# Optimization experiments

Hardware: AMD Instinct MI355X
Metric: run time of the kernel (lower is better)

The kernel has to match this reference:

```python
import jax, jax.numpy as jnp
import numpy as np

V, D, H, DH, DI, L = 10000, 512, 8, 64, 2048, 12
B, S = 4, 1024
MAX_KLEN = 1024 + 0 + 512  # tgt_len + ext_len + mem_len
EPS = 1e-5
STD = 0.02


def setup_inputs() -> dict:
    key = jax.random.key(0)
    ks = jax.random.split(key, 10)
    data = jax.random.randint(ks[0], (B, S), 0, V)
    word_emb = jax.random.normal(ks[1], (V, D), jnp.float32) * STD
    pos_emb = jax.random.normal(ks[2], (MAX_KLEN, D), jnp.float32) * STD
    Wq = jax.random.normal(ks[3], (L, H * DH, D), jnp.float32) * STD
    Wkv = jax.random.normal(ks[4], (L, 2 * H * DH, D), jnp.float32) * STD
    Wo = jax.random.normal(ks[5], (L, D, H * DH), jnp.float32) * STD
    ln1_g = jnp.ones((L, D), jnp.float32)
    ln1_b = jnp.zeros((L, D), jnp.float32)
    W1 = jax.random.normal(ks[6], (L, DI, D), jnp.float32) * STD
    b1 = jnp.zeros((L, DI), jnp.float32)
    W2 = jax.random.normal(ks[7], (L, D, DI), jnp.float32) * STD
    b2 = jnp.zeros((L, D), jnp.float32)
    ln2_g = jnp.ones((L, D), jnp.float32)
    ln2_b = jnp.zeros((L, D), jnp.float32)
    out_b = jnp.zeros((V,), jnp.float32)  # out_layer weight is tied to word_emb
    return dict(data=data, word_emb=word_emb, pos_emb=pos_emb, Wq=Wq, Wkv=Wkv,
                Wo=Wo, ln1_g=ln1_g, ln1_b=ln1_b, W1=W1, b1=b1, W2=W2, b2=b2,
                ln2_g=ln2_g, ln2_b=ln2_b, out_b=out_b)


def _layernorm(x, g, b):
    m = jnp.mean(x, axis=-1, keepdims=True)
    v = jnp.mean((x - m) ** 2, axis=-1, keepdims=True)
    return (x - m) * jax.lax.rsqrt(v + EPS) * g + b


def reference(data, word_emb, pos_emb, Wq, Wkv, Wo, ln1_g, ln1_b,
              W1, b1, W2, b2, ln2_g, ln2_b, out_b):
    # mems start empty -> mlen = 0, klen = qlen, standard causal mask.
    h = word_emb[data] + pos_emb[:S][None, :, :]      # [B, S, D]
    mask = jnp.triu(jnp.ones((S, S), bool), 1)        # True above diagonal
    scale = 1.0 / np.sqrt(DH)

    def layer(h, p):
        wq, wkv, wo, g1, bl1, w1, bf1, w2, bf2, g2, bl2 = p
        q = (h @ wq.T).reshape(B, S, H, DH)
        k, v = jnp.split(h @ wkv.T, 2, axis=-1)
        k = k.reshape(B, S, H, DH)
        v = v.reshape(B, S, H, DH)
        sc = jnp.einsum('bqhd,bkhd->bhqk', q, k) * scale
        sc = jnp.where(mask[None, None], -jnp.inf, sc)
        p_attn = jax.nn.softmax(sc, axis=-1)           # [B, H, S, S] materialized
        av = jnp.einsum('bhqk,bkhd->bqhd', p_attn, v).reshape(B, S, H * DH)
        h = _layernorm(h + av @ wo.T, g1, bl1)         # post-LN (pre_lnorm=False)
        ff = jax.nn.relu(h @ w1.T + bf1) @ w2.T + bf2
        h = _layernorm(h + ff, g2, bl2)
        return h, None

    h, _ = jax.lax.scan(layer, h,
                        (Wq, Wkv, Wo, ln1_g, ln1_b, W1, b1, W2, b2, ln2_g, ln2_b))
    logits = h @ word_emb.T + out_b                    # tied output projection
    return logits                                      # [B, S, V]
```

## Files before the change

### kernel.cpp

```cpp
#include <hip/hip_runtime.h>

#define VV 10000
#define DD 512
#define HH 8
#define DH 64
#define DI 2048
#define LL 12
#define BB 4
#define SS 1024
#define TT (BB * SS)


typedef __attribute__((ext_vector_type(8))) short bhalf8;
typedef __attribute__((ext_vector_type(16))) float f32x16;

__device__ __forceinline__ void split_bf16(float x, unsigned short& h, unsigned short& l)
{
    unsigned int u = __float_as_uint(x);
    unsigned int r = (u + 0x7FFFu + ((u >> 16) & 1u)) & 0xFFFF0000u;
    h = (unsigned short)(r >> 16);
    float lf = x - __uint_as_float(r);
    unsigned int ul = __float_as_uint(lf);
    l = (unsigned short)((ul + 0x7FFFu + ((ul >> 16) & 1u)) >> 16);
}

__global__ __launch_bounds__(256) void convsplit(
    const float* __restrict__ src, unsigned short* __restrict__ hi,
    unsigned short* __restrict__ lo, int n4)
{
    int stride = gridDim.x * 256;
    for (int i = blockIdx.x * 256 + threadIdx.x; i < n4; i += stride) {
        float4 v = ((const float4*)src)[i];
        ushort4 h, l;
        split_bf16(v.x, h.x, l.x);
        split_bf16(v.y, h.y, l.y);
        split_bf16(v.z, h.z, l.z);
        split_bf16(v.w, h.w, l.w);
        ((ushort4*)hi)[i] = h;
        ((ushort4*)lo)[i] = l;
    }
}

__global__ __launch_bounds__(256) void embed_kernel(
    const int* __restrict__ data, const float* __restrict__ we,
    const float* __restrict__ pe, float* __restrict__ h,
    unsigned short* __restrict__ hhi, unsigned short* __restrict__ hlo)
{
    int tok = blockIdx.x;
    int tid = threadIdx.x;
    int idx = data[tok];
    int s = tok & (SS - 1);
    size_t base = (size_t)tok * DD;
    size_t wb = (size_t)idx * DD;
    size_t pb = (size_t)s * DD;
    float a = we[wb + tid] + pe[pb + tid];
    float b = we[wb + 256 + tid] + pe[pb + 256 + tid];
    h[base + tid] = a;
    h[base + 256 + tid] = b;
    unsigned short hx, lx;
    split_bf16(a, hx, lx); hhi[base + tid] = hx;       hlo[base + tid] = lx;
    split_bf16(b, hx, lx); hhi[base + 256 + tid] = hx; hlo[base + 256 + tid] = lx;
}

template<int BN, int EPI, bool SWZ>
__global__ __launch_bounds__(256) void gemm_mfma(
    const unsigned short* __restrict__ Ahp, const unsigned short* __restrict__ Alp,
    const unsigned short* __restrict__ Whp, const unsigned short* __restrict__ Wlp,
    const float* __restrict__ bias, float* __restrict__ C,
    unsigned short* __restrict__ Chp, unsigned short* __restrict__ Clp,
    unsigned short* __restrict__ Vhp, unsigned short* __restrict__ Vlp,
    int N, int K)
{
    constexpr int FN  = BN / 64;
    constexpr int BT  = BN * 128;
    constexpr int NBG = BN / 8;
    constexpr int NGRP = 32 + 2 * NBG;
    constexpr int PW  = NGRP / 4;
    __shared__ __align__(16) char smem[32768 + 2 * BT];

    int bx = blockIdx.x, by = blockIdx.y;
    if (SWZ) {
        int id = by * 79 + bx;
        int t  = (id & 7) * 316 + (id >> 3);
        if (t < 2240) { int c = t / 320, r = t - c * 320; by = r / 10; bx = c * 10 + r % 10; }
        else          { int r = t - 2240;                 by = r / 9;  bx = 70 + r % 9; }
    }

    const int tid   = threadIdx.x;
    const int lane  = tid & 63;
    const int wid   = tid >> 6;
    const int wm    = wid >> 1;
    const int wn    = wid & 1;
    const int laneM = lane & 31;
    const int laneK = lane >> 5;
    const int m0    = by * 128;
    const int n0    = bx * BN;
    const int srow8 = lane >> 3;
    const int sslot = lane & 7;

    const int dAl = (int)(Alp - Ahp);
    const int dW  = (int)(Whp - Ahp);
    const int dWl = (int)(Wlp - Ahp);
    int offs[PW];
    int ldso[PW];
    #pragma unroll
    for (int t = 0; t < PW; ++t) {
        int g = wid * PW + t;
        if (g < 32) {
            int row = (g & 15) * 8 + srow8;
            offs[t] = (g < 16 ? 0 : dAl) + (m0 + row) * K + sslot * 8;
            ldso[t] = ((g >> 4) << 14) + sslot * 2048 + ((row ^ sslot) << 4);
        } else {
            int d = g - 32;
            int row = (d & (NBG - 1)) * 8 + srow8;
            int n = n0 + row;
            n = (n < N) ? n : (N - 1);
            offs[t] = (d < NBG ? dW : dWl) + n * K + sslot * 8;
            ldso[t] = 32768 + ((d < NBG) ? 0 : BT)
                    + sslot * (BN * 16) + ((row ^ sslot) << 4);
        }
    }

    f32x16 acc[2][FN];
    #pragma unroll
    for (int i = 0; i < 2; ++i)
        #pragma unroll
        for (int j = 0; j < FN; ++j)
            #pragma unroll
            for (int r = 0; r < 16; ++r) acc[i][j][r] = 0.f;

    bhalf8 rbuf[PW];
    #pragma unroll
    for (int t = 0; t < PW; ++t)
        rbuf[t] = *(const bhalf8*)(Ahp + offs[t]);

    for (int k0 = 0; k0 < K; k0 += 64) {
        __syncthreads();
        #pragma unroll
        for (int t = 0; t < PW; ++t)
            *(bhalf8*)(smem + ldso[t]) = rbuf[t];
        __syncthreads();

        if (k0 + 64 < K) {
            #pragma unroll
            for (int t = 0; t < PW; ++t)
                rbuf[t] = *(const bhalf8*)(Ahp + offs[t] + k0 + 64);
        }

        #pragma unroll
        for (int kb = 0; kb < 4; ++kb) {
            const int slot = kb * 2 + laneK;
            bhalf8 ah[2], al[2], bh[FN], bl[FN];
            #pragma unroll
            for (int i = 0; i < 2; ++i) {
                int row = wm * 64 + i * 32 + laneM;
                int off = slot * 2048 + ((row ^ slot) << 4);
                ah[i] = *(const bhalf8*)(smem + off);
                al[i] = *(const bhalf8*)(smem + 16384 + off);
            }
            #pragma unroll
            for (int j = 0; j < FN; ++j) {
                int row = wn * (BN / 2) + j * 32 + laneM;
                int off = 32768 + slot * (BN * 16) + ((row ^ slot) << 4);
                bh[j] = *(const bhalf8*)(smem + off);
                bl[j] = *(const bhalf8*)(smem + BT + off);
            }
            #pragma unroll
            for (int i = 0; i < 2; ++i)
                #pragma unroll
                for (int j = 0; j < FN; ++j) {
                    acc[i][j] = __builtin_amdgcn_mfma_f32_32x32x16_bf16(ah[i], bh[j], acc[i][j], 0, 0, 0);
                    acc[i][j] = __builtin_amdgcn_mfma_f32_32x32x16_bf16(ah[i], bl[j], acc[i][j], 0, 0, 0);
                    acc[i][j] = __builtin_amdgcn_mfma_f32_32x32x16_bf16(al[i], bh[j], acc[i][j], 0, 0, 0);
                }
        }
    }

    #pragma unroll
    for (int j = 0; j < FN; ++j) {
        int ncol = n0 + wn * (BN / 2) + j * 32 + laneM;
        bool nok = (ncol < N);
        float bv = 0.f;
        if (EPI == 1 || EPI == 2) { if (nok) bv = bias[ncol]; }
        #pragma unroll
        for (int i = 0; i < 2; ++i) {
            #pragma unroll
            for (int r = 0; r < 16; ++r) {
                int mrow = m0 + wm * 64 + i * 32 + (r & 3) + ((r >> 2) << 3) + laneK * 4;
                float v = acc[i][j][r] + bv;
                if (EPI == 2) v = fmaxf(v, 0.f);
                if (nok) {
                    if (EPI == 2 || EPI == 3) {
                        unsigned short hx, lx;
                        split_bf16(v, hx, lx);
                        Chp[(size_t)mrow * N + ncol] = hx;
                        Clp[(size_t)mrow * N + ncol] = lx;
                    } else if (EPI == 4) {
                        unsigned short hx, lx;
                        split_bf16(v, hx, lx);
                        if (ncol < 512) {
                            Chp[(size_t)mrow * 512 + ncol] = hx;
                            Clp[(size_t)mrow * 512 + ncol] = lx;
                        } else {
                            Vhp[(size_t)(ncol - 512) * TT + mrow] = hx;
                            Vlp[(size_t)(ncol - 512) * TT + mrow] = lx;
                        }
                    } else {
                        C[(size_t)mrow * N + ncol] = v;
                    }
                }
            }
        }
    }
}

__global__ __launch_bounds__(128) void flash_mfma(
    const unsigned short* __restrict__ qhp, const unsigned short* __restrict__ qlp,
    const unsigned short* __restrict__ khp, const unsigned short* __restrict__ klp,
    const unsigned short* __restrict__ vthp, const unsigned short* __restrict__ vtlp,
    unsigned short* __restrict__ avh, unsigned short* __restrict__ avl)
{
    __shared__ __align__(16) char lds[50176];

    const int qt  = 15 - (int)blockIdx.x;
    const int hh  = blockIdx.y;
    const int b   = blockIdx.z;
    const int tid = threadIdx.x;
    const int lane  = tid & 63;
    const int wq    = tid >> 6;
    const int laneM = lane & 31;
    const int laneK = lane >> 5;
    const int q0    = qt * 64;

    bhalf8 Qh[4], Ql[4];
    {
        size_t qoff = (size_t)(b * SS + q0 + 32 * wq + laneM) * 512 + hh * 64 + 8 * laneK;
        #pragma unroll
        for (int ks = 0; ks < 4; ++ks) {
            Qh[ks] = *(const bhalf8*)(qhp + qoff + 16 * ks);
            Ql[ks] = *(const bhalf8*)(qlp + qoff + 16 * ks);
        }
    }

    f32x16 O0, O1;
    #pragma unroll
    for (int r = 0; r < 16; ++r) { O0[r] = 0.f; O1[r] = 0.f; }
    float mrun = -1e30f, lrun = 0.f;

    const int srow  = tid >> 1;
    const int shalf = tid & 1;
    float* Pl = (float*)(lds + 32768 + wq * 8704);

    for (int kt = 0; kt <= qt; ++kt) {
        __syncthreads();
        {
            size_t kbase = (size_t)(b * SS + kt * 64 + srow) * 512 + hh * 64 + 32 * shalf;
            size_t vbase = (size_t)(hh * 64 + srow) * TT + b * SS + kt * 64 + 32 * shalf;
            bhalf8 k0[4], k1[4], v0[4], v1[4];
            #pragma unroll
            for (int j = 0; j < 4; ++j) {
                k0[j] = *(const bhalf8*)(khp  + kbase + 8 * j);
                k1[j] = *(const bhalf8*)(klp  + kbase + 8 * j);
                v0[j] = *(const bhalf8*)(vthp + vbase + 8 * j);
                v1[j] = *(const bhalf8*)(vtlp + vbase + 8 * j);
            }
            int ob = srow * 128 + 64 * shalf;
            int sw = (srow & 7) << 4;
            #pragma unroll
            for (int j = 0; j < 4; ++j) {
                int o = (ob + 16 * j) ^ sw;
                *(bhalf8*)(lds + o)         = k0[j];
                *(bhalf8*)(lds + 8192 + o)  = k1[j];
                *(bhalf8*)(lds + 16384 + o) = v0[j];
                *(bhalf8*)(lds + 24576 + o) = v1[j];
            }
        }
        __syncthreads();

        f32x16 s0, s1;
        #pragma unroll
        for (int r = 0; r < 16; ++r) { s0[r] = 0.f; s1[r] = 0.f; }
        __builtin_amdgcn_s_setprio(1);
        #pragma unroll
        for (int ks = 0; ks < 4; ++ks) {
            int db = 32 * ks + 16 * laneK;
            int o0 = (laneM * 128 + db) ^ ((laneM & 7) << 4);
            int r1 = 32 + laneM;
            int o1 = (r1 * 128 + db) ^ ((r1 & 7) << 4);
            bhalf8 kh0 = *(const bhalf8*)(lds + o0);
            bhalf8 kl0 = *(const bhalf8*)(lds + 8192 + o0);
            bhalf8 kh1 = *(const bhalf8*)(lds + o1);
            bhalf8 kl1 = *(const bhalf8*)(lds + 8192 + o1);
            s0 = __builtin_amdgcn_mfma_f32_32x32x16_bf16(kh0, Qh[ks], s0, 0, 0, 0);
            s0 = __builtin_amdgcn_mfma_f32_32x32x16_bf16(kh0, Ql[ks], s0, 0, 0, 0);
            s0 = __builtin_amdgcn_mfma_f32_32x32x16_bf16(kl0, Qh[ks], s0, 0, 0, 0);
            s1 = __builtin_amdgcn_mfma_f32_32x32x16_bf16(kh1, Qh[ks], s1, 0, 0, 0);
            s1 = __builtin_amdgcn_mfma_f32_32x32x16_bf16(kh1, Ql[ks], s1, 0, 0, 0);
            s1 = __builtin_amdgcn_mfma_f32_32x32x16_bf16(kl1, Qh[ks], s1, 0, 0, 0);
        }
        __builtin_amdgcn_s_setprio(0);

        #pragma unroll
        for (int r = 0; r < 16; ++r) { s0[r] *= 0.125f; s1[r] *= 0.125f; }

        if (kt == qt) {
            int qrel = 32 * wq + laneM;
            #pragma unroll
            for (int r = 0; r < 16; ++r) {
                int krel = (r & 3) + ((r >> 2) << 3) + 4 * laneK;
                if (krel > qrel)      s0[r] = -1e30f;
                if (krel + 32 > qrel) s1[r] = -1e30f;
            }
        }

        float mx = s0[0];
        #pragma unroll
        for (int r = 1; r < 16; ++r) mx = fmaxf(mx, s0[r]);
        #pragma unroll
        for (int r = 0; r < 16; ++r) mx = fmaxf(mx, s1[r]);
        mx = fmaxf(mx, __shfl_xor(mx, 32));
        float mn = fmaxf(mrun, mx);
        float alpha = __expf(mrun - mn);
        mrun = mn;
        float rs = 0.f;
        #pragma unroll
        for (int r = 0; r < 16; ++r) {
            float p0 = __expf(s0[r] - mn);
            float p1 = __expf(s1[r] - mn);
            s0[r] = p0; s1[r] = p1;
            rs += p0 + p1;
        }
        rs += __shfl_xor(rs, 32);
        lrun = lrun * alpha + rs;
        #pragma unroll
        for (int r = 0; r < 16; ++r) { O0[r] *= alpha; O1[r] *= alpha; }

        #pragma unroll
        for (int r = 0; r < 16; ++r) {
            int krel = (r & 3) + ((r >> 2) << 3) + 4 * laneK;
            Pl[laneM * 68 + krel]      = s0[r];
            Pl[laneM * 68 + 32 + krel] = s1[r];
        }
        __asm__ volatile("s_waitcnt lgkmcnt(0)" ::: "memory");
        __builtin_amdgcn_sched_barrier(0);

        #pragma unroll
        for (int ks = 0; ks < 4; ++ks) {
            const float* pr = &Pl[laneM * 68 + 16 * ks + 8 * laneK];
            float4 pa = *(const float4*)pr;
            float4 pb = *(const float4*)(pr + 4);
            float pv[8] = {pa.x, pa.y, pa.z, pa.w, pb.x, pb.y, pb.z, pb.w};
            bhalf8 ph, plo;
            #pragma unroll
            for (int i = 0; i < 8; ++i) {
                unsigned u = __float_as_uint(pv[i]);
                ph[i] = (short)(u >> 16);
                float lf = pv[i] - __uint_as_float(u & 0xFFFF0000u);
                plo[i] = (short)(__float_as_uint(lf) >> 16);
            }
            int db = 32 * ks + 16 * laneK;
            __builtin_amdgcn_s_setprio(1);
            {
                int col = laneM;
                int o = (col * 128 + db) ^ ((col & 7) << 4);
                bhalf8 vh = *(const bhalf8*)(lds + 16384 + o);
                bhalf8 vl = *(const bhalf8*)(lds + 24576 + o);
                O0 = __builtin_amdgcn_mfma_f32_32x32x16_bf16(vh, ph,  O0, 0, 0, 0);
                O0 = __builtin_amdgcn_mfma_f32_32x32x16_bf16(vl, ph,  O0, 0, 0, 0);
                O0 = __builtin_amdgcn_mfma_f32_32x32x16_bf16(vh, plo, O0, 0, 0, 0);
            }
            {
                int col = 32 + laneM;
                int o = (col * 128 + db) ^ ((col & 7) << 4);
                bhalf8 vh = *(const bhalf8*)(lds + 16384 + o);
                bhalf8 vl = *(const bhalf8*)(lds + 24576 + o);
                O1 = __builtin_amdgcn_mfma_f32_32x32x16_bf16(vh, ph,  O1, 0, 0, 0);
                O1 = __builtin_amdgcn_mfma_f32_32x32x16_bf16(vl, ph,  O1, 0, 0, 0);
                O1 = __builtin_amdgcn_mfma_f32_32x32x16_bf16(vh, plo, O1, 0, 0, 0);
            }
            __builtin_amdgcn_s_setprio(0);
        }
    }

    float inv = 1.0f / lrun;
    #pragma unroll
    for (int r = 0; r < 16; ++r) {
        int d = (r & 3) + ((r >> 2) << 3) + 4 * laneK;
        Pl[laneM * 68 + d]      = O0[r] * inv;
        Pl[laneM * 68 + 32 + d] = O1[r] * inv;
    }
    __asm__ volatile("s_waitcnt lgkmcnt(0)" ::: "memory");
    __builtin_amdgcn_sched_barrier(0);
    #pragma unroll
    for (int it = 0; it < 16; ++it) {
        int qr = it * 2 + (lane >> 5);
        int d  = (lane & 31) * 2;
        float2 v = *(const float2*)&Pl[qr * 68 + d];
        unsigned short h0, l0, h1, l1;
        split_bf16(v.x, h0, l0);
        split_bf16(v.y, h1, l1);
        size_t base = (size_t)(b * SS + q0 + 32 * wq + qr) * 512 + hh * 64 + d;
        ushort2 hv; hv.x = h0; hv.y = h1;
        ushort2 lv; lv.x = l0; lv.y = l1;
        *(ushort2*)(avh + base) = hv;
        *(ushort2*)(avl + base) = lv;
    }
}

__global__ __launch_bounds__(256) void add_ln_kernel(
    float* __restrict__ h, const float* __restrict__ x,
    const float* __restrict__ g, const float* __restrict__ bta,
    unsigned short* __restrict__ hhi, unsigned short* __restrict__ hlo)
{
    int tok = blockIdx.x, tid = threadIdx.x;
    size_t base = (size_t)tok * DD;
    float v0 = h[base + tid] + x[base + tid];
    float v1 = h[base + 256 + tid] + x[base + 256 + tid];

    __shared__ float rs[256], rq[256];
    rs[tid] = v0 + v1;
    rq[tid] = v0 * v0 + v1 * v1;
    __syncthreads();
    for (int off = 128; off > 0; off >>= 1) {
        if (tid < off) { rs[tid] += rs[tid + off]; rq[tid] += rq[tid + off]; }
        __syncthreads();
    }
    float mean = rs[0] * (1.f / 512.f);
    float var  = rq[0] * (1.f / 512.f) - mean * mean;
    float inv  = rsqrtf(var + 1e-5f);
    float o0 = (v0 - mean) * inv * g[tid]       + bta[tid];
    float o1 = (v1 - mean) * inv * g[256 + tid] + bta[256 + tid];
    h[base + tid]       = o0;
    h[base + 256 + tid] = o1;
    unsigned short a, b;
    split_bf16(o0, a, b); hhi[base + tid]       = a; hlo[base + tid]       = b;
    split_bf16(o1, a, b); hhi[base + 256 + tid] = a; hlo[base + 256 + tid] = b;
}

extern "C" void kernel_launch(void* const* d_in, const int* in_sizes, int n_in,
                              void* d_out, int out_size, void* d_ws, size_t ws_size,
                              hipStream_t stream)
{
    const int*   data = (const int*)d_in[0];
    const float* we   = (const float*)d_in[1];
    const float* pe   = (const float*)d_in[2];
    const float* Wq   = (const float*)d_in[3];
    const float* Wkv  = (const float*)d_in[4];
    const float* Wo   = (const float*)d_in[5];
    const float* g1   = (const float*)d_in[6];
    const float* bl1  = (const float*)d_in[7];
    const float* W1   = (const float*)d_in[8];
    const float* b1   = (const float*)d_in[9];
    const float* W2   = (const float*)d_in[10];
    const float* b2   = (const float*)d_in[11];
    const float* g2   = (const float*)d_in[12];
    const float* bl2  = (const float*)d_in[13];
    const float* outb = (const float*)d_in[14];
    float* out = (float*)d_out;

    typedef unsigned short us;
    float* h    = (float*)d_ws;
    us* qhp  = (us*)(h + (size_t)TT * 512);
    us* qlp  = qhp  + (size_t)TT * 512;
    us* khp  = qlp  + (size_t)TT * 512;
    us* klp  = khp  + (size_t)TT * 512;
    us* vthp = klp  + (size_t)TT * 512;
    us* vtlp = vthp + (size_t)TT * 512;
    us* avh  = vtlp + (size_t)TT * 512;
    us* avl  = avh  + (size_t)TT * 512;
    float* tmp = (float*)(avl + (size_t)TT * 512);
    us* hhi  = (us*)(tmp + (size_t)TT * 512);
    us* hlo  = hhi + (size_t)TT * 512;
    us* ffh = qhp;
    us* ffl = qhp + (size_t)TT * 2048;
    us* wqh  = hlo + (size_t)TT * 512;
    us* wql  = wqh  + (size_t)LL * 512 * 512;
    us* wkvh = wql  + (size_t)LL * 512 * 512;
    us* wkvl = wkvh + (size_t)LL * 1024 * 512;
    us* woh  = wkvl + (size_t)LL * 1024 * 512;
    us* wol  = woh  + (size_t)LL * 512 * 512;
    us* w1h  = wol  + (size_t)LL * 512 * 512;
    us* w1l  = w1h  + (size_t)LL * 2048 * 512;
    us* w2h  = w1l  + (size_t)LL * 2048 * 512;
    us* w2l  = w2h  + (size_t)LL * 512 * 2048;
    us* weh  = w2l  + (size_t)LL * 512 * 2048;
    us* wel  = weh  + (size_t)VV * 512;

    auto cv = [&](const float* s, us* hh, us* ll, size_t n) {
        int n4 = (int)(n >> 2);
        int blocks = (n4 + 255) / 256;
        if (blocks > 2048) blocks = 2048;
        convsplit<<<blocks, 256, 0, stream>>>(s, hh, ll, n4);
    };
    cv(Wq,  wqh,  wql,  (size_t)LL * 512 * 512);
    cv(Wkv, wkvh, wkvl, (size_t)LL * 1024 * 512);
    cv(Wo,  woh,  wol,  (size_t)LL * 512 * 512);
    cv(W1,  w1h,  w1l,  (size_t)LL * 2048 * 512);
    cv(W2,  w2h,  w2l,  (size_t)LL * 512 * 2048);
    cv(we,  weh,  wel,  (size_t)VV * 512);

    embed_kernel<<<TT, 256, 0, stream>>>(data, we, pe, h, hhi, hlo);

    for (int l = 0; l < LL; ++l) {
        const us* lwqh  = wqh  + (size_t)l * 512 * 512;
        const us* lwql  = wql  + (size_t)l * 512 * 512;
        const us* lwkvh = wkvh + (size_t)l * 1024 * 512;
        const us* lwkvl = wkvl + (size_t)l * 1024 * 512;
        const us* lwoh  = woh  + (size_t)l * 512 * 512;
        const us* lwol  = wol  + (size_t)l * 512 * 512;
        const us* lw1h  = w1h  + (size_t)l * 2048 * 512;
        const us* lw1l  = w1l  + (size_t)l * 2048 * 512;
        const us* lw2h  = w2h  + (size_t)l * 512 * 2048;
        const us* lw2l  = w2l  + (size_t)l * 512 * 2048;

        gemm_mfma<64, 3, false><<<dim3(8, 32), 256, 0, stream>>>(
            hhi, hlo, lwqh, lwql, nullptr, nullptr, qhp, qlp, nullptr, nullptr, 512, 512);
        gemm_mfma<128, 4, false><<<dim3(8, 32), 256, 0, stream>>>(
            hhi, hlo, lwkvh, lwkvl, nullptr, nullptr, khp, klp, vthp, vtlp, 1024, 512);
        flash_mfma<<<dim3(16, HH, BB), 128, 0, stream>>>(
            qhp, qlp, khp, klp, vthp, vtlp, avh, avl);
        gemm_mfma<64, 0, false><<<dim3(8, 32), 256, 0, stream>>>(
            avh, avl, lwoh, lwol, nullptr, tmp, nullptr, nullptr, nullptr, nullptr, 512, 512);
        add_ln_kernel<<<TT, 256, 0, stream>>>(h, tmp, g1 + l * 512, bl1 + l * 512, hhi, hlo);
        gemm_mfma<128, 2, false><<<dim3(16, 32), 256, 0, stream>>>(
            hhi, hlo, lw1h, lw1l, b1 + l * 2048, nullptr, ffh, ffl, nullptr, nullptr, 2048, 512);
        gemm_mfma<64, 1, false><<<dim3(8, 32), 256, 0, stream>>>(
            ffh, ffl, lw2h, lw2l, b2 + l * 512, tmp, nullptr, nullptr, nullptr, nullptr, 512, 2048);
        add_ln_kernel<<<TT, 256, 0, stream>>>(h, tmp, g2 + l * 512, bl2 + l * 512, hhi, hlo);
    }

    gemm_mfma<128, 1, true><<<dim3((VV + 127) / 128, 32), 256, 0, stream>>>(
        hhi, hlo, weh, wel, outb, out, nullptr, nullptr, nullptr, nullptr, VV, 512);
}
```

Before: 3.218 ms.

## Fuse Q/K/V projections into one GEMM and add deeper prefetch for N=512 GEMMs

Packs Wq and Wkv into one concatenated split-bf16 weight, so the Q, K and V projections run as a single GEMM launch with an epilogue that routes columns to Q (pre-scaled by 1/sqrt(DH)), K, and transposed V. The softmax scale multiply is removed from the flash kernel. A DEEP=2 option holds two register prefetch buffers, giving the Wo and W2 GEMMs a longer gap between issuing a global load and storing it to LDS. This cuts one launch per layer and improves occupancy for the projection GEMM, at the cost of more registers in the double-prefetch variant.

After: 2.900 ms. 1.11x faster.

```diff
diff --git a/kernel.cpp b/kernel.cpp
--- a/kernel.cpp
+++ b/kernel.cpp
@@ -38,6 +38,31 @@
         split_bf16(v.w, h.w, l.w);
         ((ushort4*)hi)[i] = h;
         ((ushort4*)lo)[i] = l;
+    }
+}
+
+__global__ __launch_bounds__(256) void packqkv(
+    const float* __restrict__ Wq, const float* __restrict__ Wkv,
+    unsigned short* __restrict__ hi, unsigned short* __restrict__ lo)
+{
+    const int total = LL * 1536 * 128;
+    int stride = gridDim.x * 256;
+    for (int i = blockIdx.x * 256 + threadIdx.x; i < total; i += stride) {
+        int l   = i / (1536 * 128);
+        int rem = i - l * (1536 * 128);
+        int n   = rem >> 7;
+        int k4  = rem & 127;
+        const float* src = (n < 512)
+            ? Wq  + ((size_t)(l * 512 + n) * 512 + k4 * 4)
+            : Wkv + ((size_t)(l * 1024 + (n - 512)) * 512 + k4 * 4);
+        float4 v = *(const float4*)src;
+        ushort4 h, s;
+        split_bf16(v.x, h.x, s.x);
+        split_bf16(v.y, h.y, s.y);
+        split_bf16(v.z, h.z, s.z);
+        split_bf16(v.w, h.w, s.w);
+        ((ushort4*)hi)[i] = h;
+        ((ushort4*)lo)[i] = s;
     }
 }
 
@@ -62,12 +87,13 @@
     split_bf16(b, hx, lx); hhi[base + 256 + tid] = hx; hlo[base + 256 + tid] = lx;
 }
 
-template<int BN, int EPI, bool SWZ>
+template<int BN, int EPI, bool SWZ, int DEEP>
 __global__ __launch_bounds__(256) void gemm_mfma(
     const unsigned short* __restrict__ Ahp, const unsigned short* __restrict__ Alp,
     const unsigned short* __restrict__ Whp, const unsigned short* __restrict__ Wlp,
     const float* __restrict__ bias, float* __restrict__ C,
     unsigned short* __restrict__ Chp, unsigned short* __restrict__ Clp,
+    unsigned short* __restrict__ Khp, unsigned short* __restrict__ Klp,
     unsigned short* __restrict__ Vhp, unsigned short* __restrict__ Vlp,
     int N, int K)
 {
@@ -129,24 +155,17 @@
             #pragma unroll
             for (int r = 0; r < 16; ++r) acc[i][j][r] = 0.f;
 
-    bhalf8 rbuf[PW];
-    #pragma unroll
-    for (int t = 0; t < PW; ++t)
-        rbuf[t] = *(const bhalf8*)(Ahp + offs[t]);
-
-    for (int k0 = 0; k0 < K; k0 += 64) {
-        __syncthreads();
+    auto loadt = [&](bhalf8* rb, int k) {
         #pragma unroll
         for (int t = 0; t < PW; ++t)
-            *(bhalf8*)(smem + ldso[t]) = rbuf[t];
-        __syncthreads();
-
-        if (k0 + 64 < K) {
-            #pragma unroll
-            for (int t = 0; t < PW; ++t)
-                rbuf[t] = *(const bhalf8*)(Ahp + offs[t] + k0 + 64);
-        }
-
+            rb[t] = *(const bhalf8*)(Ahp + offs[t] + k);
+    };
+    auto stage = [&](const bhalf8* rb) {
+        #pragma unroll
+        for (int t = 0; t < PW; ++t)
+            *(bhalf8*)(smem + ldso[t]) = rb[t];
+    };
+    auto mfma_step = [&]() {
         #pragma unroll
         for (int kb = 0; kb < 4; ++kb) {
             const int slot = kb * 2 + laneK;
@@ -173,6 +192,33 @@
                     acc[i][j] = __builtin_amdgcn_mfma_f32_32x32x16_bf16(ah[i], bl[j], acc[i][j], 0, 0, 0);
                     acc[i][j] = __builtin_amdgcn_mfma_f32_32x32x16_bf16(al[i], bh[j], acc[i][j], 0, 0, 0);
                 }
+        }
+    };
+
+    bhalf8 r0[PW], r1[DEEP == 2 ? PW : 1];
+    loadt(r0, 0);
+    if (DEEP == 2) loadt(r1, 64);
+
+    if (DEEP == 1) {
+        for (int k0 = 0; k0 < K; k0 += 64) {
+            __syncthreads();
+            stage(r0);
+            __syncthreads();
+            if (k0 + 64 < K) loadt(r0, k0 + 64);
+            mfma_step();
+        }
+    } else {
+        for (int k0 = 0; k0 < K; k0 += 128) {
+            __syncthreads();
+            stage(r0);
+            __syncthreads();
+            if (k0 + 128 < K) loadt(r0, k0 + 128);
+            mfma_step();
+            __syncthreads();
+            stage(r1);
+            __syncthreads();
+            if (k0 + 192 < K) loadt(r1, k0 + 192);
+            mfma_step();
         }
     }
 
@@ -195,15 +241,20 @@
                         split_bf16(v, hx, lx);
                         Chp[(size_t)mrow * N + ncol] = hx;
                         Clp[(size_t)mrow * N + ncol] = lx;
-                    } else if (EPI == 4) {
+                    } else if (EPI == 5) {
                         unsigned short hx, lx;
-                        split_bf16(v, hx, lx);
                         if (ncol < 512) {
+                            split_bf16(v * 0.125f, hx, lx);
                             Chp[(size_t)mrow * 512 + ncol] = hx;
                             Clp[(size_t)mrow * 512 + ncol] = lx;
+                        } else if (ncol < 1024) {
+                            split_bf16(v, hx, lx);
+                            Khp[(size_t)mrow * 512 + (ncol - 512)] = hx;
+                            Klp[(size_t)mrow * 512 + (ncol - 512)] = lx;
                         } else {
-                            Vhp[(size_t)(ncol - 512) * TT + mrow] = hx;
-                            Vlp[(size_t)(ncol - 512) * TT + mrow] = lx;
+                            split_bf16(v, hx, lx);
+                            Vhp[(size_t)(ncol - 1024) * TT + mrow] = hx;
+                            Vlp[(size_t)(ncol - 1024) * TT + mrow] = lx;
                         }
                     } else {
                         C[(size_t)mrow * N + ncol] = v;
@@ -299,9 +350,6 @@
             s1 = __builtin_amdgcn_mfma_f32_32x32x16_bf16(kl1, Qh[ks], s1, 0, 0, 0);
         }
         __builtin_amdgcn_s_setprio(0);
-
-        #pragma unroll
-        for (int r = 0; r < 16; ++r) { s0[r] *= 0.125f; s1[r] *= 0.125f; }
 
         if (kt == qt) {
             int qrel = 32 * wq + laneM;
@@ -473,11 +521,9 @@
     us* hlo  = hhi + (size_t)TT * 512;
     us* ffh = qhp;
     us* ffl = qhp + (size_t)TT * 2048;
-    us* wqh  = hlo + (size_t)TT * 512;
-    us* wql  = wqh  + (size_t)LL * 512 * 512;
-    us* wkvh = wql  + (size_t)LL * 512 * 512;
-    us* wkvl = wkvh + (size_t)LL * 1024 * 512;
-    us* woh  = wkvl + (size_t)LL * 1024 * 512;
+    us* wqkvh = hlo  + (size_t)TT * 512;
+    us* wqkvl = wqkvh + (size_t)LL * 1536 * 512;
+    us* woh  = wqkvl + (size_t)LL * 1536 * 512;
     us* wol  = woh  + (size_t)LL * 512 * 512;
     us* w1h  = wol  + (size_t)LL * 512 * 512;
     us* w1l  = w1h  + (size_t)LL * 2048 * 512;
@@ -492,8 +538,7 @@
         if (blocks > 2048) blocks = 2048;
         convsplit<<<blocks, 256, 0, stream>>>(s, hh, ll, n4);
     };
-    cv(Wq,  wqh,  wql,  (size_t)LL * 512 * 512);
-    cv(Wkv, wkvh, wkvl, (size_t)LL * 1024 * 512);
+    packqkv<<<2048, 256, 0, stream>>>(Wq, Wkv, wqkvh, wqkvl);
     cv(Wo,  woh,  wol,  (size_t)LL * 512 * 512);
     cv(W1,  w1h,  w1l,  (size_t)LL * 2048 * 512);
     cv(W2,  w2h,  w2l,  (size_t)LL * 512 * 2048);
@@ -502,10 +547,8 @@
     embed_kernel<<<TT, 256, 0, stream>>>(data, we, pe, h, hhi, hlo);
 
     for (int l = 0; l < LL; ++l) {
-        const us* lwqh  = wqh  + (size_t)l * 512 * 512;
-        const us* lwql  = wql  + (size_t)l * 512 * 512;
-        const us* lwkvh = wkvh + (size_t)l * 1024 * 512;
-        const us* lwkvl = wkvl + (size_t)l * 1024 * 512;
+        const us* lwqkvh = wqkvh + (size_t)l * 1536 * 512;
+        const us* lwqkvl = wqkvl + (size_t)l * 1536 * 512;
         const us* lwoh  = woh  + (size_t)l * 512 * 512;
         const us* lwol  = wol  + (size_t)l * 512 * 512;
         const us* lw1h  = w1h  + (size_t)l * 2048 * 512;
@@ -513,22 +556,25 @@
         const us* lw2h  = w2h  + (size_t)l * 512 * 2048;
         const us* lw2l  = w2l  + (size_t)l * 512 * 2048;
 
-        gemm_mfma<64, 3, false><<<dim3(8, 32), 256, 0, stream>>>(
-            hhi, hlo, lwqh, lwql, nullptr, nullptr, qhp, qlp, nullptr, nullptr, 512, 512);
-        gemm_mfma<128, 4, false><<<dim3(8, 32), 256, 0, stream>>>(
-            hhi, hlo, lwkvh, lwkvl, nullptr, nullptr, khp, klp, vthp, vtlp, 1024, 512);
+        gemm_mfma<64, 5, false, 1><<<dim3(24, 32), 256, 0, stream>>>(
+            hhi, hlo, lwqkvh, lwqkvl, nullptr, nullptr,
+            qhp, qlp, khp, klp, vthp, vtlp, 1536, 512);
         flash_mfma<<<dim3(16, HH, BB), 128, 0, stream>>>(
             qhp, qlp, khp, klp, vthp, vtlp, avh, avl);
-        gemm_mfma<64, 0, false><<<dim3(8, 32), 256, 0, stream>>>(
-            avh, avl, lwoh, lwol, nullptr, tmp, nullptr, nullptr, nullptr, nullptr, 512, 512);
+        gemm_mfma<64, 0, false, 2><<<dim3(8, 32), 256, 0, stream>>>(
+            avh, avl, lwoh, lwol, nullptr, tmp,
+            nullptr, nullptr, nullptr, nullptr, nullptr, nullptr, 512, 512);
         add_ln_kernel<<<TT, 256, 0, stream>>>(h, tmp, g1 + l * 512, bl1 + l * 512, hhi, hlo);
-        gemm_mfma<128, 2, false><<<dim3(16, 32), 256, 0, stream>>>(
-            hhi, hlo, lw1h, lw1l, b1 + l * 2048, nullptr, ffh, ffl, nullptr, nullptr, 2048, 512);
-        gemm_mfma<64, 1, false><<<dim3(8, 32), 256, 0, stream>>>(
-            ffh, ffl, lw2h, lw2l, b2 + l * 512, tmp, nullptr, nullptr, nullptr, nullptr, 512, 2048);
+        gemm_mfma<128, 2, false, 1><<<dim3(16, 32), 256, 0, stream>>>(
+            hhi, hlo, lw1h, lw1l, b1 + l * 2048, nullptr,
+            ffh, ffl, nullptr, nullptr, nullptr, nullptr, 2048, 512);
+        gemm_mfma<64, 1, false, 2><<<dim3(8, 32), 256, 0, stream>>>(
+            ffh, ffl, lw2h, lw2l, b2 + l * 512, tmp,
+            nullptr, nullptr, nullptr, nullptr, nullptr, nullptr, 512, 2048);
         add_ln_kernel<<<TT, 256, 0, stream>>>(h, tmp, g2 + l * 512, bl2 + l * 512, hhi, hlo);
     }
 
-    gemm_mfma<128, 1, true><<<dim3((VV + 127) / 128, 32), 256, 0, stream>>>(
-        hhi, hlo, weh, wel, outb, out, nullptr, nullptr, nullptr, nullptr, VV, 512);
-}
+    gemm_mfma<128, 1, true, 1><<<dim3((VV + 127) / 128, 32), 256, 0, stream>>>(
+        hhi, hlo, weh, wel, outb, out,
+        nullptr, nullptr, nullptr, nullptr, nullptr, nullptr, VV, 512);
+}
```
